# Kernel optimization log

Hardware: AMD Instinct MI355X
Metric: run time of the kernel (lower is better)

Reference implementation:

```python
import jax, jax.numpy as jnp
import numpy as np

NUM_USER = 1000
NUM_NODES = 3000
NUM_REL = 5
HID = 500
OUT = 75
NUM_BASIS = 2
NUM_EDGES = 200000


def setup_inputs() -> dict:
    key = jax.random.key(0)
    ks = jax.random.split(key, 8)
    x = jnp.arange(NUM_NODES, dtype=jnp.int64 if jax.config.jax_enable_x64 else jnp.int32)
    edge_index = jax.random.randint(ks[0], (2, NUM_EDGES), 0, NUM_NODES)
    edge_type = jax.random.randint(ks[1], (NUM_EDGES,), 0, NUM_REL)
    edge_norm = jax.random.uniform(ks[2], (NUM_EDGES,), dtype=jnp.float32)
    # RGC ordinal basis weights: W_r = cumsum of per-relation bases (GCMC ordinal weight sharing)
    ord_basis = 0.01 * jax.random.normal(ks[3], (NUM_REL, NUM_NODES, HID), dtype=jnp.float32)
    # DenseLayer weight (no bias), shared for user/item branches
    W_dense = 0.05 * jax.random.normal(ks[4], (HID, OUT), dtype=jnp.float32)
    # BiDecoder basis decomposition
    basis_matrix = 0.1 * jax.random.normal(ks[5], (NUM_BASIS, OUT * OUT), dtype=jnp.float32)
    coefs = 0.1 * jax.random.normal(ks[6], (NUM_REL, NUM_BASIS), dtype=jnp.float32)
    return {"x": x, "edge_index": edge_index, "edge_type": edge_type,
            "edge_norm": edge_norm, "ord_basis": ord_basis, "W_dense": W_dense,
            "basis_matrix": basis_matrix, "coefs": coefs}


def reference(x, edge_index, edge_type, edge_norm, ord_basis, W_dense, basis_matrix, coefs):
    R, N, H = ord_basis.shape
    # --- RGCLayer: ordinal cumulative weight sharing ---
    weight = jnp.cumsum(ord_basis, axis=0).reshape(R * N, H)  # (R*N, H)
    src, dst = edge_index[0], edge_index[1]
    idx = edge_type * N + x[src]                      # row lookup = one-hot feature matmul
    msgs = weight[idx] * edge_norm[:, None]           # (E, H) gather, memory-bound
    agg = jax.ops.segment_sum(msgs, dst, num_segments=N)  # scatter-add to target nodes
    feat = jax.nn.relu(agg)                           # (N, H)
    # --- separate users / items, DenseLayer ---
    u = jax.nn.relu(feat[:NUM_USER] @ W_dense)        # (U, OUT)
    i = jax.nn.relu(feat[NUM_USER:] @ W_dense)        # (I, OUT)
    # --- BiDecoder: basis-combination bilinear scores per relation ---
    D = W_dense.shape[1]
    Q = jnp.einsum('rb,bk->rk', coefs, basis_matrix).reshape(R, D, D)
    out = jnp.einsum('ud,rde,ie->uir', u, Q, i)       # (U, I, R)
    return out.reshape(u.shape[0] * i.shape[0], R)
```

## Files before the change

### kernel.cpp

```cpp
#include <hip/hip_runtime.h>
#include <hip/hip_bf16.h>

#define NUSER 1000
#define NNODES 3000
#define NREL 5
#define HID 500
#define DOUT 75
#define NBASIS 2
#define NEDGES 200000
#define NITEM (NNODES - NUSER)
#define NH (NNODES * HID)
#define ROWF4 125

__global__ void k_cumsum(const float4* __restrict__ basis, float4* __restrict__ weight,
                         int* __restrict__ deg) {
    int i = blockIdx.x * blockDim.x + threadIdx.x;
    if (i < NNODES) deg[i] = 0;
    if (i >= NH / 4) return;
    float4 s = make_float4(0.f, 0.f, 0.f, 0.f);
#pragma unroll
    for (int r = 0; r < NREL; ++r) {
        float4 b = basis[r * (NH / 4) + i];
        s.x += b.x; s.y += b.y; s.z += b.z; s.w += b.w;
        weight[r * (NH / 4) + i] = s;
    }
}

__global__ void k_degree(const int* __restrict__ dst, int* __restrict__ deg) {
    int e = blockIdx.x * blockDim.x + threadIdx.x;
    if (e < NEDGES) atomicAdd(&deg[dst[e]], 1);
}

__global__ __launch_bounds__(1024) void k_scan(const int* __restrict__ deg,
                                               int* __restrict__ offs,
                                               int* __restrict__ cursor) {
    __shared__ int wsum[16];
    int t = threadIdx.x;
    int base = t * 3;
    int a = (base     < NNODES) ? deg[base]     : 0;
    int b = (base + 1 < NNODES) ? deg[base + 1] : 0;
    int c = (base + 2 < NNODES) ? deg[base + 2] : 0;
    int s = a + b + c;
    int lane = t & 63, wid = t >> 6;
    int v = s;
#pragma unroll
    for (int d = 1; d < 64; d <<= 1) {
        int x = __shfl_up(v, d);
        if (lane >= d) v += x;
    }
    if (lane == 63) wsum[wid] = v;
    __syncthreads();
    if (t < 16) {
        int w = wsum[t];
#pragma unroll
        for (int d = 1; d < 16; d <<= 1) {
            int x = __shfl_up(w, d);
            if (t >= d) w += x;
        }
        wsum[t] = w;
    }
    __syncthreads();
    int woff = wid ? wsum[wid - 1] : 0;
    int incl = v + woff;
    int excl = incl - s;
    if (base < NNODES)     { offs[base]     = excl;         cursor[base]     = excl; }
    if (base + 1 < NNODES) { offs[base + 1] = excl + a;     cursor[base + 1] = excl + a; }
    if (base + 2 < NNODES) { offs[base + 2] = excl + a + b; cursor[base + 2] = excl + a + b; }
    if (t == 1023) offs[NNODES] = incl;
}

__global__ void k_fill(const int* __restrict__ src, const int* __restrict__ dst,
                       const int* __restrict__ etype, const float* __restrict__ enorm,
                       const int* __restrict__ x,
                       int* __restrict__ cursor, int* __restrict__ csr_row,
                       float* __restrict__ csr_norm) {
    int e = blockIdx.x * blockDim.x + threadIdx.x;
    if (e >= NEDGES) return;
    int d = dst[e];
    int pos = atomicAdd(&cursor[d], 1);
    csr_row[pos] = etype[e] * NNODES + x[src[e]];
    csr_norm[pos] = enorm[e];
}

__global__ __launch_bounds__(256) void k_agg(const float4* __restrict__ w4,
                                             const int* __restrict__ offs,
                                             const int* __restrict__ csr_row,
                                             const float* __restrict__ csr_norm,
                                             float4* __restrict__ feat4) {
    int bid = blockIdx.x;
    int s = bid & 7;
    int chunk = bid >> 3;
    int t = threadIdx.x;
    int g = t >> 4;
    int lane = t & 15;
    int n = chunk * 16 + g;
    if (n >= NNODES) return;
    int wdt = (s < 7) ? 16 : 13;
    int boff = s * 16;
    int beg = offs[n], end = offs[n + 1];
    bool act = lane < wdt;
    float4 acc = make_float4(0.f, 0.f, 0.f, 0.f);
#pragma unroll 4
    for (int p = beg; p < end; ++p) {
        int row = csr_row[p];
        float wn = csr_norm[p];
        if (act) {
            float4 v = w4[(size_t)row * ROWF4 + boff + lane];
            acc.x += v.x * wn; acc.y += v.y * wn;
            acc.z += v.z * wn; acc.w += v.w * wn;
        }
    }
    if (act) {
        acc.x = fmaxf(acc.x, 0.f); acc.y = fmaxf(acc.y, 0.f);
        acc.z = fmaxf(acc.z, 0.f); acc.w = fmaxf(acc.w, 0.f);
        feat4[(size_t)n * ROWF4 + boff + lane] = acc;
    }
}

#define DN 8
__global__ __launch_bounds__(256) void k_dense(const float* __restrict__ feat,
                                               const float* __restrict__ W,
                                               float* __restrict__ uv) {
    __shared__ float lds[DN][HID];
    int nb = blockIdx.x * DN;
    int t = threadIdx.x;
    const float4* f4 = (const float4*)(feat + (size_t)nb * HID);
    float4* l4 = (float4*)&lds[0][0];
    for (int j = t; j < DN * HID / 4; j += 256) l4[j] = f4[j];
    __syncthreads();
    if (t < 225) {
        int g = t / 75, o = t % 75;
        float a0 = 0.f, a1 = 0.f, a2 = 0.f;
        for (int d = 0; d < HID; ++d) {
            float w = W[d * DOUT + o];
            a0 += lds[g][d] * w;
            a1 += lds[g + 3][d] * w;
            a2 += lds[(g + 6) & 7][d] * w;
        }
        uv[(nb + g) * DOUT + o]     = fmaxf(a0, 0.f);
        uv[(nb + g + 3) * DOUT + o] = fmaxf(a1, 0.f);
        if (g < 2) uv[(nb + g + 6) * DOUT + o] = fmaxf(a2, 0.f);
    }
}

__global__ void k_T(const float* __restrict__ uv, const float* __restrict__ bm,
                    float* __restrict__ T) {
    int i = blockIdx.x * blockDim.x + threadIdx.x;
    if (i >= NBASIS * NUSER * DOUT) return;
    int b = i / (NUSER * DOUT);
    int rem = i % (NUSER * DOUT);
    int u = rem / DOUT;
    int e = rem % DOUT;
    float acc = 0.f;
    for (int d = 0; d < DOUT; ++d)
        acc += uv[u * DOUT + d] * bm[b * DOUT * DOUT + d * DOUT + e];
    T[i] = acc;
}

#define UT 32
#define IT 128
#define EC 25
__global__ __launch_bounds__(256) void k_dec(const float* __restrict__ T,
                                             const float* __restrict__ uv,
                                             const float* __restrict__ coefs,
                                             float* __restrict__ out) {
    __shared__ float As[NBASIS][UT][EC];
    __shared__ float Is[IT][EC];
    int t = threadIdx.x;
    int ti = t & 31;
    int tu = t >> 5;
    int ub = blockIdx.y * UT;
    int ib = blockIdx.x * IT;

    float acc[NBASIS][4][4] = {};

    for (int e0 = 0; e0 < DOUT; e0 += EC) {
        for (int j = t; j < NBASIS * UT * EC; j += 256) {
            int b = j / (UT * EC);
            int rem = j % (UT * EC);
            int uu = rem / EC, c = rem % EC;
            int u = ub + uu;
            As[b][uu][c] = (u < NUSER) ? T[(b * NUSER + u) * DOUT + e0 + c] : 0.f;
        }
        for (int j = t; j < IT * EC; j += 256) {
            int ii = j / EC, c = j % EC;
            int i = ib + ii;
            Is[ii][c] = (i < NITEM) ? uv[(size_t)(NUSER + i) * DOUT + e0 + c] : 0.f;
        }
        __syncthreads();
        for (int c = 0; c < EC; ++c) {
            float av[NBASIS][4];
#pragma unroll
            for (int b = 0; b < NBASIS; ++b)
#pragma unroll
                for (int uu = 0; uu < 4; ++uu)
                    av[b][uu] = As[b][tu * 4 + uu][c];
            float iv[4];
#pragma unroll
            for (int k = 0; k < 4; ++k) iv[k] = Is[ti + 32 * k][c];
#pragma unroll
            for (int b = 0; b < NBASIS; ++b)
#pragma unroll
                for (int uu = 0; uu < 4; ++uu)
#pragma unroll
                    for (int k = 0; k < 4; ++k)
                        acc[b][uu][k] += av[b][uu] * iv[k];
        }
        __syncthreads();
    }

    float cf[NREL][NBASIS];
#pragma unroll
    for (int r = 0; r < NREL; ++r)
#pragma unroll
        for (int b = 0; b < NBASIS; ++b) cf[r][b] = coefs[r * NBASIS + b];

#pragma unroll
    for (int uu = 0; uu < 4; ++uu) {
        int u = ub + tu * 4 + uu;
        if (u >= NUSER) continue;
#pragma unroll
        for (int k = 0; k < 4; ++k) {
            int i = ib + ti + 32 * k;
            if (i >= NITEM) continue;
            size_t base = ((size_t)u * NITEM + i) * NREL;
            float s0 = acc[0][uu][k], s1 = acc[1][uu][k];
#pragma unroll
            for (int r = 0; r < NREL; ++r)
                out[base + r] = cf[r][0] * s0 + cf[r][1] * s1;
        }
    }
}

extern "C" void kernel_launch(void* const* d_in, const int* in_sizes, int n_in,
                              void* d_out, int out_size, void* d_ws, size_t ws_size,
                              hipStream_t stream) {
    const int*   x     = (const int*)d_in[0];
    const int*   ei    = (const int*)d_in[1];
    const int*   etype = (const int*)d_in[2];
    const float* enorm = (const float*)d_in[3];
    const float* basis = (const float*)d_in[4];
    const float* Wd    = (const float*)d_in[5];
    const float* bm    = (const float*)d_in[6];
    const float* coefs = (const float*)d_in[7];
    float* out = (float*)d_out;

    float* weight   = (float*)d_ws;
    float* feat     = weight + 7500000;
    float* uv       = feat + 1500000;
    float* T        = uv + 225000;
    float* csr_norm = T + 150000;
    int*   csr_row  = (int*)(csr_norm + 200000);
    int*   deg      = csr_row + 200000;
    int*   offs     = deg + 3000;
    int*   cursor   = offs + 3001;

    const int* src = ei;
    const int* dst = ei + NEDGES;

    k_cumsum<<<(NH / 4 + 255) / 256, 256, 0, stream>>>((const float4*)basis,
                                                       (float4*)weight, deg);
    k_degree<<<(NEDGES + 255) / 256, 256, 0, stream>>>(dst, deg);
    k_scan<<<1, 1024, 0, stream>>>(deg, offs, cursor);
    k_fill<<<(NEDGES + 255) / 256, 256, 0, stream>>>(src, dst, etype, enorm, x, cursor,
                                                     csr_row, csr_norm);
    k_agg<<<((NNODES + 15) / 16) * 8, 256, 0, stream>>>((const float4*)weight, offs,
                                                        csr_row, csr_norm, (float4*)feat);
    k_dense<<<NNODES / DN, 256, 0, stream>>>(feat, Wd, uv);
    k_T<<<(NBASIS * NUSER * DOUT + 255) / 256, 256, 0, stream>>>(uv, bm, T);
    k_dec<<<dim3((NITEM + IT - 1) / IT, (NUSER + UT - 1) / UT), 256, 0, stream>>>(T, uv, coefs, out);
}
```

Before: 272.1 us.

## Fuse degree count into scan, split edges per node across wave, fuse dense with T

Degree counting moves into the single-block scan kernel using shared-memory atomics, which removes the separate degree kernel and the deg zeroing. The aggregation kernel now gives each node a full 64-lane wave whose four 16-lane groups handle every fourth edge, with partial sums combined by xor shuffles. This aims to raise memory-level parallelism for the gather. The T projection is folded into the dense kernel through shared memory, removing one launch. Risks: a single block now does 200k atomics serially in one CU, and the extra reductions add shuffle overhead.

```diff
diff --git a/kernel.cpp b/kernel.cpp
--- a/kernel.cpp
+++ b/kernel.cpp
@@ -12,10 +12,8 @@
 #define NH (NNODES * HID)
 #define ROWF4 125
 
-__global__ void k_cumsum(const float4* __restrict__ basis, float4* __restrict__ weight,
-                         int* __restrict__ deg) {
+__global__ void k_cumsum(const float4* __restrict__ basis, float4* __restrict__ weight) {
     int i = blockIdx.x * blockDim.x + threadIdx.x;
-    if (i < NNODES) deg[i] = 0;
     if (i >= NH / 4) return;
     float4 s = make_float4(0.f, 0.f, 0.f, 0.f);
 #pragma unroll
@@ -26,20 +24,20 @@
     }
 }
 
-__global__ void k_degree(const int* __restrict__ dst, int* __restrict__ deg) {
-    int e = blockIdx.x * blockDim.x + threadIdx.x;
-    if (e < NEDGES) atomicAdd(&deg[dst[e]], 1);
-}
-
-__global__ __launch_bounds__(1024) void k_scan(const int* __restrict__ deg,
-                                               int* __restrict__ offs,
-                                               int* __restrict__ cursor) {
+__global__ __launch_bounds__(1024) void k_csr(const int* __restrict__ dst,
+                                              int* __restrict__ offs,
+                                              int* __restrict__ cursor) {
+    __shared__ int cnt[NNODES];
     __shared__ int wsum[16];
     int t = threadIdx.x;
+    for (int j = t; j < NNODES; j += 1024) cnt[j] = 0;
+    __syncthreads();
+    for (int e = t; e < NEDGES; e += 1024) atomicAdd(&cnt[dst[e]], 1);
+    __syncthreads();
     int base = t * 3;
-    int a = (base     < NNODES) ? deg[base]     : 0;
-    int b = (base + 1 < NNODES) ? deg[base + 1] : 0;
-    int c = (base + 2 < NNODES) ? deg[base + 2] : 0;
+    int a = (base     < NNODES) ? cnt[base]     : 0;
+    int b = (base + 1 < NNODES) ? cnt[base + 1] : 0;
+    int c = (base + 2 < NNODES) ? cnt[base + 2] : 0;
     int s = a + b + c;
     int lane = t & 63, wid = t >> 6;
     int v = s;
@@ -91,26 +89,32 @@
     int s = bid & 7;
     int chunk = bid >> 3;
     int t = threadIdx.x;
-    int g = t >> 4;
-    int lane = t & 15;
-    int n = chunk * 16 + g;
-    if (n >= NNODES) return;
+    int w = t >> 6;
+    int l = t & 63;
+    int g = l >> 4;
+    int lane = l & 15;
+    int n = chunk * 4 + w;
     int wdt = (s < 7) ? 16 : 13;
     int boff = s * 16;
     int beg = offs[n], end = offs[n + 1];
     bool act = lane < wdt;
+    const float4* wp = w4 + boff + lane;
     float4 acc = make_float4(0.f, 0.f, 0.f, 0.f);
-#pragma unroll 4
-    for (int p = beg; p < end; ++p) {
+#pragma unroll 2
+    for (int p = beg + g; p < end; p += 4) {
         int row = csr_row[p];
         float wn = csr_norm[p];
         if (act) {
-            float4 v = w4[(size_t)row * ROWF4 + boff + lane];
+            float4 v = wp[(size_t)row * ROWF4];
             acc.x += v.x * wn; acc.y += v.y * wn;
             acc.z += v.z * wn; acc.w += v.w * wn;
         }
     }
-    if (act) {
+    acc.x += __shfl_xor(acc.x, 16); acc.y += __shfl_xor(acc.y, 16);
+    acc.z += __shfl_xor(acc.z, 16); acc.w += __shfl_xor(acc.w, 16);
+    acc.x += __shfl_xor(acc.x, 32); acc.y += __shfl_xor(acc.y, 32);
+    acc.z += __shfl_xor(acc.z, 32); acc.w += __shfl_xor(acc.w, 32);
+    if (g == 0 && act) {
         acc.x = fmaxf(acc.x, 0.f); acc.y = fmaxf(acc.y, 0.f);
         acc.z = fmaxf(acc.z, 0.f); acc.w = fmaxf(acc.w, 0.f);
         feat4[(size_t)n * ROWF4 + boff + lane] = acc;
@@ -118,10 +122,13 @@
 }
 
 #define DN 8
-__global__ __launch_bounds__(256) void k_dense(const float* __restrict__ feat,
-                                               const float* __restrict__ W,
-                                               float* __restrict__ uv) {
+__global__ __launch_bounds__(256) void k_denseT(const float* __restrict__ feat,
+                                                const float* __restrict__ W,
+                                                const float* __restrict__ bm,
+                                                float* __restrict__ uv,
+                                                float* __restrict__ T) {
     __shared__ float lds[DN][HID];
+    __shared__ float uvs[DN][DOUT + 1];
     int nb = blockIdx.x * DN;
     int t = threadIdx.x;
     const float4* f4 = (const float4*)(feat + (size_t)nb * HID);
@@ -137,24 +144,23 @@
             a1 += lds[g + 3][d] * w;
             a2 += lds[(g + 6) & 7][d] * w;
         }
-        uv[(nb + g) * DOUT + o]     = fmaxf(a0, 0.f);
-        uv[(nb + g + 3) * DOUT + o] = fmaxf(a1, 0.f);
-        if (g < 2) uv[(nb + g + 6) * DOUT + o] = fmaxf(a2, 0.f);
-    }
-}
-
-__global__ void k_T(const float* __restrict__ uv, const float* __restrict__ bm,
-                    float* __restrict__ T) {
-    int i = blockIdx.x * blockDim.x + threadIdx.x;
-    if (i >= NBASIS * NUSER * DOUT) return;
-    int b = i / (NUSER * DOUT);
-    int rem = i % (NUSER * DOUT);
-    int u = rem / DOUT;
-    int e = rem % DOUT;
-    float acc = 0.f;
-    for (int d = 0; d < DOUT; ++d)
-        acc += uv[u * DOUT + d] * bm[b * DOUT * DOUT + d * DOUT + e];
-    T[i] = acc;
+        a0 = fmaxf(a0, 0.f); a1 = fmaxf(a1, 0.f); a2 = fmaxf(a2, 0.f);
+        uv[(nb + g) * DOUT + o]     = a0;  uvs[g][o]     = a0;
+        uv[(nb + g + 3) * DOUT + o] = a1;  uvs[g + 3][o] = a1;
+        if (g < 2) { uv[(nb + g + 6) * DOUT + o] = a2; uvs[g + 6][o] = a2; }
+    }
+    if (nb >= NUSER) return;
+    __syncthreads();
+    for (int j = t; j < NBASIS * DN * DOUT; j += 256) {
+        int b = j / (DN * DOUT);
+        int rem = j % (DN * DOUT);
+        int ul = rem / DOUT, e = rem % DOUT;
+        const float* bp = bm + b * DOUT * DOUT + e;
+        float acc = 0.f;
+        for (int d = 0; d < DOUT; ++d)
+            acc += uvs[ul][d] * bp[d * DOUT];
+        T[((size_t)b * NUSER + nb + ul) * DOUT + e] = acc;
+    }
 }
 
 #define UT 32
@@ -180,7 +186,7 @@
             int rem = j % (UT * EC);
             int uu = rem / EC, c = rem % EC;
             int u = ub + uu;
-            As[b][uu][c] = (u < NUSER) ? T[(b * NUSER + u) * DOUT + e0 + c] : 0.f;
+            As[b][uu][c] = (u < NUSER) ? T[((size_t)b * NUSER + u) * DOUT + e0 + c] : 0.f;
         }
         for (int j = t; j < IT * EC; j += 256) {
             int ii = j / EC, c = j % EC;
@@ -251,22 +257,19 @@
     float* T        = uv + 225000;
     float* csr_norm = T + 150000;
     int*   csr_row  = (int*)(csr_norm + 200000);
-    int*   deg      = csr_row + 200000;
-    int*   offs     = deg + 3000;
+    int*   offs     = csr_row + 200000;
     int*   cursor   = offs + 3001;
 
     const int* src = ei;
     const int* dst = ei + NEDGES;
 
     k_cumsum<<<(NH / 4 + 255) / 256, 256, 0, stream>>>((const float4*)basis,
-                                                       (float4*)weight, deg);
-    k_degree<<<(NEDGES + 255) / 256, 256, 0, stream>>>(dst, deg);
-    k_scan<<<1, 1024, 0, stream>>>(deg, offs, cursor);
+                                                       (float4*)weight);
+    k_csr<<<1, 1024, 0, stream>>>(dst, offs, cursor);
     k_fill<<<(NEDGES + 255) / 256, 256, 0, stream>>>(src, dst, etype, enorm, x, cursor,
                                                      csr_row, csr_norm);
-    k_agg<<<((NNODES + 15) / 16) * 8, 256, 0, stream>>>((const float4*)weight, offs,
-                                                        csr_row, csr_norm, (float4*)feat);
-    k_dense<<<NNODES / DN, 256, 0, stream>>>(feat, Wd, uv);
-    k_T<<<(NBASIS * NUSER * DOUT + 255) / 256, 256, 0, stream>>>(uv, bm, T);
+    k_agg<<<(NNODES / 4) * 8, 256, 0, stream>>>((const float4*)weight, offs,
+                                                csr_row, csr_norm, (float4*)feat);
+    k_denseT<<<NNODES / DN, 256, 0, stream>>>(feat, Wd, bm, uv, T);
     k_dec<<<dim3((NITEM + IT - 1) / IT, (NUSER + UT - 1) / UT), 256, 0, stream>>>(T, uv, coefs, out);
 }
```

Result: slower. 320.0 us (+17.6%).
